# Optimization experiments

Measured on AMD Instinct MI355X. Metric: run time of the kernel, lower is better.

The kernel has to match this reference:

```python
import jax, jax.numpy as jnp
import numpy as np

# ---- hyperparameters (mirror the module's globals) ----
SZ      = 4096   # batch
SENLEN  = 128    # sentence length
VOCAB   = 50000  # len(wordVec)
DWE     = 100    # dimWE
MAXPOS  = 256    # MaxPos
DPE     = 5      # dimPE
DIMR    = 40     # dimR (event/role vocab)
DEE     = 32     # dimEE
DRE     = 16     # dimRE
MAXE    = 9      # maxE
DC      = 128    # dimC_arg
LOCLEN  = 16     # words in `loc` per sample
CIN     = DWE + 2 * DPE + DEE + (MAXE - 1) * DRE  # 270


def setup_inputs() -> dict:
    ks = jax.random.split(jax.random.key(0), 16)
    inp      = jax.random.randint(ks[0], (SZ, SENLEN), 0, VOCAB)
    pos1     = jax.random.randint(ks[1], (SZ, SENLEN), 0, MAXPOS)
    pos2     = jax.random.randint(ks[2], (SZ, SENLEN), 0, MAXPOS)
    loc      = jax.random.randint(ks[3], (SZ, LOCLEN), 0, VOCAB)
    # loc_mark in [1, 11] so indices 4:4+mark and 4+mark stay inside LOCLEN=16
    loc_mark = jax.random.randint(ks[4], (SZ,), 1, 12)
    subtype  = jax.random.randint(ks[5], (SZ,), 0, DIMR)
    argRole  = jax.random.randint(ks[6], (SZ, MAXE - 1), 0, DIMR)
    # binary piecewise masks (left / middle / right of the two anchors)
    maskL = (jax.random.uniform(ks[7], (SZ, SENLEN)) > 0.5).astype(jnp.float32)
    maskM = (jax.random.uniform(ks[8], (SZ, SENLEN)) > 0.5).astype(jnp.float32)
    maskR = (jax.random.uniform(ks[9], (SZ, SENLEN)) > 0.5).astype(jnp.float32)
    # learned parameters
    word_emb  = (jax.random.normal(ks[10], (VOCAB, DWE)) * 0.02).at[0].set(0.0)  # padding_idx=0
    pos_emb   = jax.random.normal(ks[11], (MAXPOS, DPE)) * 0.02
    event_emb = (jax.random.normal(ks[12], (DIMR, DEE)) * 0.02).at[0].set(0.0)
    role_emb  = (jax.random.normal(ks[13], (DIMR, DRE)) * 0.02).at[0].set(0.0)
    conv_w    = jax.random.normal(ks[14], (DC, CIN, 3)) * 0.02  # (out, in, k)
    conv_b    = jax.random.normal(ks[15], (DC,)) * 0.02
    return dict(inp=inp, pos1=pos1, pos2=pos2, loc=loc, loc_mark=loc_mark,
                subtype=subtype, argRole=argRole, maskL=maskL, maskM=maskM,
                maskR=maskR, word_emb=word_emb, pos_emb=pos_emb,
                event_emb=event_emb, role_emb=role_emb, conv_w=conv_w,
                conv_b=conv_b)


def reference(inp, pos1, pos2, loc, loc_mark, subtype, argRole,
              maskL, maskM, maskR, word_emb, pos_emb, event_emb, role_emb,
              conv_w, conv_b):
    sz = inp.shape[0]
    embeds = word_emb[inp]            # [SZ, S, DWE]
    p1 = pos_emb[pos1]                # [SZ, S, DPE]
    p2 = pos_emb[pos2]                # [SZ, S, DPE]

    # ---- vectorized ragged loc pooling (replaces the per-sample loop) ----
    loc_e = word_emb[loc]             # [SZ, LOCLEN, DWE]
    csum  = jnp.cumsum(loc_e, axis=1)
    # mean of loc_e[4 : 4+mark]  = (csum[3+mark] - csum[3]) / mark
    upper = jnp.take_along_axis(csum, (3 + loc_mark)[:, None, None], axis=1)[:, 0]
    mean4 = (upper - csum[:, 3]) / loc_mark[:, None].astype(loc_e.dtype)
    l5    = jnp.take_along_axis(loc_e, (4 + loc_mark)[:, None, None], axis=1)[:, 0]
    loc_embeds = jnp.concatenate(
        [loc_e[:, :4].reshape(sz, -1), mean4, l5], axis=1)  # [SZ, 6*DWE]

    # event / role embeddings broadcast across the sentence
    ev = jnp.broadcast_to(event_emb[subtype][:, None, :], (sz, SENLEN, DEE))
    rl = jnp.broadcast_to(role_emb[argRole].reshape(sz, 1, -1),
                          (sz, SENLEN, (MAXE - 1) * DRE))

    x = jnp.concatenate([embeds, p1, p2, ev, rl], axis=2)  # [SZ, S, CIN]
    x = jnp.transpose(x, (0, 2, 1))                         # [SZ, CIN, S]
    conved = jax.lax.conv_general_dilated(
        x, conv_w, window_strides=(1,), padding=[(1, 1)],
        dimension_numbers=('NCH', 'OIH', 'NCH')) + conv_b[None, :, None]

    def piece_pool(m):  # masked +1 then max over sentence
        return jnp.max(conved * m[:, None, :] + 1.0, axis=2)  # [SZ, DC]

    pooled = jnp.concatenate(
        [piece_pool(maskL), piece_pool(maskM), piece_pool(maskR)], axis=1) - 1.0
    rep = jnp.tanh(jnp.concatenate([pooled, loc_embeds], axis=1))  # dropout = identity (eval)
    return rep
```

## Files before the change

### kernel.cpp

```cpp
#include <hip/hip_runtime.h>
#include <hip/hip_bf16.h>

typedef unsigned short u16;
typedef __attribute__((ext_vector_type(8))) short bf16x8;
typedef __attribute__((ext_vector_type(4))) float f32x4;
typedef __attribute__((ext_vector_type(4))) int i32x4;
typedef __attribute__((ext_vector_type(2))) unsigned int u32x2;

constexpr int SEN  = 128;
constexpr int CIN  = 270;
constexpr int KA   = 352;
constexpr int NOUT = 984;
constexpr int XROW = 256;
constexpr int XTB  = 130 * XROW;
constexpr int WEBP = 256;
constexpr size_t WS_BASE = 90112 + 61440 + 491520;
constexpr size_t WS_NEED = WS_BASE + 50000ull * WEBP;

__device__ inline float ftanh(float x) {
    float e = __expf(2.0f * x);
    return 1.0f - 2.0f * __builtin_amdgcn_rcpf(e + 1.0f);
}
__device__ inline unsigned pk2(float x, float y) {
    union { __hip_bfloat162 h; unsigned u; } v;
    v.h = __float22bfloat162_rn(float2{x, y});
    return v.u;
}
__device__ __forceinline__ void gload_lds16(const void* g, void* l) {
    __builtin_amdgcn_global_load_lds(
        (const __attribute__((address_space(1))) void*)g,
        (__attribute__((address_space(3))) void*)l, 16, 0, 0);
}

__global__ void prep_all(const float* __restrict__ w, const float* __restrict__ ee,
                         const float* __restrict__ re, const int* __restrict__ loc,
                         const int* __restrict__ lmark, const float* __restrict__ we,
                         u16* __restrict__ Av, float* __restrict__ SE3,
                         float* __restrict__ SR3, u16* __restrict__ weB,
                         float* __restrict__ out) {
    const int b = blockIdx.x, tid = threadIdx.x;
    if (b < 176) {
        int i = b * 256 + tid;
        int dc = i / KA, K = i - dc * KA;
        int tap = (K >= 112) + (K >= 224) + (K >= 336);
        int ch  = K - 112 * tap;
        float v = (tap < 3 && ch < 110) ? w[(dc * CIN + ch) * 3 + tap] : 0.0f;
        union { __hip_bfloat16 h; u16 u; } cv;
        cv.h = __float2bfloat16(v);
        Av[i] = cv.u;
    } else if (b < 236) {
        int i = (b - 176) * 256 + tid;
        int k = i % 3, rest = i / 3;
        int dc = rest & 127, e = rest >> 7;
        float a = 0.f;
        for (int j = 0; j < 32; ++j)
            a += w[(dc * CIN + 110 + j) * 3 + k] * ee[e * 32 + j];
        SE3[i] = a;
    } else if (b < 716) {
        int i = (b - 236) * 256 + tid;
        int k = i % 3, rest = i / 3;
        int dc = rest & 127, rr = rest >> 7;
        int r = rr % 40, j = rr / 40;
        float a = 0.f;
        for (int d = 0; d < 16; ++d)
            a += w[(dc * CIN + 142 + j * 16 + d) * 3 + k] * re[r * 16 + d];
        SR3[i] = a;
    } else if (b < 2764) {
        int li = b - 716;
        int s = li * 2 + (tid >> 7);
        int d = tid & 127;
        if (d < 100) {
            const int* L = loc + (size_t)s * 16;
            float* o = out + (size_t)s * NOUT + 384;
#pragma unroll
            for (int i = 0; i < 4; ++i)
                o[i * 100 + d] = ftanh(we[(size_t)L[i] * 100 + d]);
            int mk = lmark[s];
            float acc = 0.f;
            for (int j = 0; j < mk; ++j)
                acc += we[(size_t)L[4 + j] * 100 + d];
            o[4 * 100 + d] = ftanh(acc / (float)mk);
            o[5 * 100 + d] = ftanh(we[(size_t)L[4 + mk] * 100 + d]);
        }
    } else {
        size_t i = (size_t)(b - 2764) * 256 + tid;
        int v  = (int)(i >> 6), cp = (int)(i & 63);
        int c0 = cp * 2;
        float x0 = (c0     < 100) ? we[(size_t)v * 100 + c0]     : 0.f;
        float x1 = (c0 + 1 < 100) ? we[(size_t)v * 100 + c0 + 1] : 0.f;
        ((unsigned*)weB)[(size_t)v * 64 + cp] = pk2(x0, x1);
    }
}

template <bool GLD>
__global__ __launch_bounds__(512)
__attribute__((amdgpu_waves_per_eu(4)))
void conv_pool(const int* __restrict__ inp, const int* __restrict__ pos1,
               const int* __restrict__ pos2, const int* __restrict__ subtype,
               const int* __restrict__ argRole,
               const float* __restrict__ maskL, const float* __restrict__ maskM,
               const float* __restrict__ maskR,
               const float* __restrict__ we, const float* __restrict__ pe,
               const float* __restrict__ cb,
               const u16* __restrict__ Av, const float* __restrict__ SE3,
               const float* __restrict__ SR3, const u16* __restrict__ weB,
               float* __restrict__ out)
{
    __shared__ __align__(16) char xT[2][XTB];
    __shared__ float sc[2][3 * 128];
    __shared__ float msk[2][3 * 128];

    const int tid  = threadIdx.x;
    const int lane = tid & 63;
    const int wid  = tid >> 6;
    const int cl   = lane & 15;
    const int rg   = lane >> 4;

    {
        i32x4 z = {0, 0, 0, 0};
        i32x4* pz = (i32x4*)xT;
#pragma unroll
        for (int i = 0; i < 9; ++i) {
            int o = tid + i * 512;
            if (o < 2 * XTB / 16) pz[o] = z;
        }
    }
    __syncthreads();

    const char* apBase = (const char*)Av + (wid * 16 + cl) * (KA * 2) + rg * 16;

    int addrB[11];
#pragma unroll
    for (int c = 0; c < 11; ++c) {
        int g   = 32 * c + 8 * rg;
        int tap = (g >= 112) + (g >= 224);
        int ch  = g - 112 * tap;
        int row0 = cl + tap;
        int phys = (ch >> 3) ^ (row0 & 15);
        addrB[c] = row0 * XROW + (phys << 4);
    }

    const int sbase = blockIdx.x * 8;

    float sk0 = 0.f, sk1 = 0.f, sk2 = 0.f;
    float cbv = (tid < 128) ? cb[tid] : 0.f;
    float pp[10];
#pragma unroll
    for (int i = 0; i < 10; ++i) pp[i] = 0.f;

    auto issueGather = [&](int s, char* xb, float* mb) {
#pragma unroll
        for (int q = 0; q < 4; ++q) {
            const int j   = (wid << 2) + q;
            const int tok = (j << 2) + (lane >> 4);
            const int idx = inp[s * SEN + tok];
            const int e   = (lane & 15) ^ ((tok + 1) & 15);
            const char* src = (const char*)weB + (size_t)idx * WEBP + (e << 4);
            gload_lds16(src, xb + XROW + (j << 10));
        }
        if (wid == 4) {
            const char* gL = (const char*)(maskL + (size_t)s * SEN);
            const char* gM = (const char*)(maskM + (size_t)s * SEN);
            const char* gR = (const char*)(maskR + (size_t)s * SEN);
            const char* s1 = (lane < 32) ? gL + (lane << 4)
                                         : gM + ((lane - 32) << 4);
            gload_lds16(s1, (char*)mb);
            if (lane < 32)
                gload_lds16(gR + (lane << 4), (char*)mb + 1024);
        }
    };

    auto smallLoad = [&](int s) {
        if (tid < 128) {
            int sub = subtype[s];
            i32x4 a0 = *(const i32x4*)(argRole + s * 8);
            i32x4 a1 = *(const i32x4*)(argRole + s * 8 + 4);
            int arr[8] = {a0[0], a0[1], a0[2], a0[3], a1[0], a1[1], a1[2], a1[3]};
            const float* bb = SE3 + (sub * 128 + tid) * 3;
            sk0 = bb[0]; sk1 = bb[1]; sk2 = bb[2];
#pragma unroll
            for (int j = 0; j < 8; ++j) {
                const float* rb = SR3 + ((j * 40 + arr[j]) * 128 + tid) * 3;
                sk0 += rb[0]; sk1 += rb[1]; sk2 += rb[2];
            }
        } else if (tid < 256) {
            int t = tid - 128;
            int p1 = pos1[s * SEN + t], p2 = pos2[s * SEN + t];
#pragma unroll
            for (int i = 0; i < 5; ++i) {
                pp[i]     = pe[p1 * 5 + i];
                pp[5 + i] = pe[p2 * 5 + i];
            }
        }
    };

    auto smallCommit = [&](int s, char* xb, float* scb, float* mb) {
        if (tid < 128) {
            scb[tid]       = sk0 + sk1 + sk2 + cbv;
            scb[128 + tid] = sk0;
            scb[256 + tid] = sk2;
        } else if (tid < 256) {
            int t = tid - 128, row = t + 1, rx = row & 15;
            u32x2 wa = { pk2(pp[0], pp[1]), pk2(pp[2], pp[3]) };
            *(u32x2*)(xb + row * XROW + ((12 ^ rx) << 4) + 8) = wa;
            union { bf16x8 v; unsigned u[4]; } wb;
            wb.u[0] = pk2(pp[4], pp[5]); wb.u[1] = pk2(pp[6], pp[7]);
            wb.u[2] = pk2(pp[8], pp[9]); wb.u[3] = 0;
            *(bf16x8*)(xb + row * XROW + ((13 ^ rx) << 4)) = wb.v;
        }
        if constexpr (!GLD) {
#pragma unroll
            for (int jj = 0; jj < 7; ++jj) {
                int q = tid + jj * 512;
                if (q < 3200) {
                    int tok = q / 25;
                    int e   = q - tok * 25;
                    int idx = inp[s * SEN + tok];
                    f32x4 v = *(const f32x4*)(we + (size_t)idx * 100 + e * 4);
                    int row  = tok + 1;
                    int phys = (e >> 1) ^ (row & 15);
                    u32x2 wv = { pk2(v[0], v[1]), pk2(v[2], v[3]) };
                    *(u32x2*)(xb + row * XROW + (phys << 4) + (e & 1) * 8) = wv;
                }
            }
            if (tid >= 256 && tid < 352) {
                int i = tid - 256;
                int m = i >> 5, j4 = i & 31;
                const float* msrc = (m == 0) ? maskL : (m == 1) ? maskM : maskR;
                *(f32x4*)(mb + m * 128 + j4 * 4) =
                    *(const f32x4*)(msrc + (size_t)s * SEN + j4 * 4);
            }
        }
    };

    smallLoad(sbase);
    if constexpr (GLD) issueGather(sbase, xT[0], msk[0]);
    __syncthreads();
    smallCommit(sbase, xT[0], sc[0], msk[0]);
    __syncthreads();

    for (int it = 0; it < 8; ++it) {
        const int s   = sbase + it;
        const int cur = it & 1;
        const char* xc = xT[cur];

        if (it < 7) {
            if constexpr (GLD) issueGather(s + 1, xT[cur ^ 1], msk[cur ^ 1]);
            smallLoad(s + 1);
        }

        const char* ap = apBase;
        asm volatile("" : "+v"(ap));

        f32x4 acc[8];
#pragma unroll
        for (int nf = 0; nf < 8; ++nf) acc[nf] = (f32x4){0.f, 0.f, 0.f, 0.f};

#pragma unroll
        for (int c = 0; c < 11; ++c) {
            const bf16x8 a = *(const bf16x8*)(ap + c * 64);
#pragma unroll
            for (int nf = 0; nf < 8; ++nf) {
                bf16x8 b = *(const bf16x8*)(xc + addrB[c] + nf * 4096);
                acc[nf] = __builtin_amdgcn_mfma_f32_16x16x32_bf16(
                    a, b, acc[nf], 0, 0, 0);
            }
        }

        const float* scc = sc[cur];
        const float* mc  = msk[cur];
        float sall[4], s0v[4], s2v[4];
#pragma unroll
        for (int r = 0; r < 4; ++r) {
            int dc = wid * 16 + rg * 4 + r;
            sall[r] = scc[dc]; s0v[r] = scc[128 + dc]; s2v[r] = scc[256 + dc];
        }
        float pm[3][4];
#pragma unroll
        for (int m = 0; m < 3; ++m)
#pragma unroll
            for (int r = 0; r < 4; ++r) pm[m][r] = -1e30f;

#pragma unroll
        for (int nf = 0; nf < 8; ++nf) {
            const int tt = nf * 16 + cl;
            const float m0 = mc[tt], m1 = mc[128 + tt], m2 = mc[256 + tt];
#pragma unroll
            for (int r = 0; r < 4; ++r) {
                float v = acc[nf][r] + sall[r];
                if (nf == 0) v -= (cl == 0)  ? s0v[r] : 0.f;
                if (nf == 7) v -= (cl == 15) ? s2v[r] : 0.f;
                pm[0][r] = fmaxf(pm[0][r], __builtin_fmaf(v, m0, 1.f));
                pm[1][r] = fmaxf(pm[1][r], __builtin_fmaf(v, m1, 1.f));
                pm[2][r] = fmaxf(pm[2][r], __builtin_fmaf(v, m2, 1.f));
            }
        }
#pragma unroll
        for (int m = 0; m < 3; ++m)
#pragma unroll
            for (int r = 0; r < 4; ++r)
#pragma unroll
                for (int d = 1; d < 16; d <<= 1)
                    pm[m][r] = fmaxf(pm[m][r], __shfl_xor(pm[m][r], d));
        if (cl < 3) {
            float* o = out + (size_t)s * NOUT + cl * 128 + wid * 16 + rg * 4;
#pragma unroll
            for (int r = 0; r < 4; ++r) {
                float v = (cl == 0) ? pm[0][r] : (cl == 1) ? pm[1][r] : pm[2][r];
                o[r] = ftanh(v - 1.f);
            }
        }

        __syncthreads();
        if (it < 7) smallCommit(s + 1, xT[cur ^ 1], sc[cur ^ 1], msk[cur ^ 1]);
        __syncthreads();
    }
}

extern "C" void kernel_launch(void* const* d_in, const int* in_sizes, int n_in,
                              void* d_out, int out_size, void* d_ws, size_t ws_size,
                              hipStream_t stream) {
    const int*   inp     = (const int*)d_in[0];
    const int*   pos1    = (const int*)d_in[1];
    const int*   pos2    = (const int*)d_in[2];
    const int*   loc     = (const int*)d_in[3];
    const int*   lmark   = (const int*)d_in[4];
    const int*   subtype = (const int*)d_in[5];
    const int*   argRole = (const int*)d_in[6];
    const float* maskL   = (const float*)d_in[7];
    const float* maskM   = (const float*)d_in[8];
    const float* maskR   = (const float*)d_in[9];
    const float* we      = (const float*)d_in[10];
    const float* pe      = (const float*)d_in[11];
    const float* ee      = (const float*)d_in[12];
    const float* re      = (const float*)d_in[13];
    const float* cw      = (const float*)d_in[14];
    const float* cb      = (const float*)d_in[15];
    float* out = (float*)d_out;

    char* ws = (char*)d_ws;
    u16*   Av  = (u16*)ws;
    float* SE3 = (float*)(ws + 90112);
    float* SR3 = (float*)(ws + 90112 + 61440);
    u16*   weB = (u16*)(ws + WS_BASE);

    const bool gld = (ws_size >= WS_NEED);
    const int prepGrid = gld ? 15264 : 2764;

    hipLaunchKernelGGL(prep_all, dim3(prepGrid), dim3(256), 0, stream,
                       cw, ee, re, loc, lmark, we, Av, SE3, SR3, weB, out);
    if (gld) {
        hipLaunchKernelGGL((conv_pool<true>), dim3(512), dim3(512), 0, stream,
                           inp, pos1, pos2, subtype, argRole, maskL, maskM, maskR,
                           we, pe, cb, Av, SE3, SR3, weB, out);
    } else {
        hipLaunchKernelGGL((conv_pool<false>), dim3(512), dim3(512), 0, stream,
                           inp, pos1, pos2, subtype, argRole, maskL, maskM, maskR,
                           we, pe, cb, Av, SE3, SR3, weB, out);
    }
}
```

Baseline: 97.80 us.

## Restructure conv GEMM to 32x32x16 MFMA with tokens as A operand

Switches the conv GEMM from 16x16x32 MFMAs (weights as A, tokens as B, each wave owning 16 output channels across all tokens) to 32x32x16 MFMAs where each wave owns 32 tokens by 64 channels, with the activation tile as the A operand. Weights are re-laid-out in prep so they are streamed from global/L2 per k-step. The piecewise max-pool now reduces partially per wave and then combines four token-quarters through a new shared-memory buffer before tanh and store. This aims to cut LDS reads per MFMA and the shuffle-heavy reduction, at the cost of an extra LDS buffer and a cross-wave reduction step.

```diff
diff --git a/kernel.cpp b/kernel.cpp
--- a/kernel.cpp
+++ b/kernel.cpp
@@ -4,12 +4,12 @@
 typedef unsigned short u16;
 typedef __attribute__((ext_vector_type(8))) short bf16x8;
 typedef __attribute__((ext_vector_type(4))) float f32x4;
+typedef __attribute__((ext_vector_type(16))) float f32x16;
 typedef __attribute__((ext_vector_type(4))) int i32x4;
 typedef __attribute__((ext_vector_type(2))) unsigned int u32x2;
 
 constexpr int SEN  = 128;
 constexpr int CIN  = 270;
-constexpr int KA   = 352;
 constexpr int NOUT = 984;
 constexpr int XROW = 256;
 constexpr int XTB  = 130 * XROW;
@@ -35,19 +35,22 @@
 __global__ void prep_all(const float* __restrict__ w, const float* __restrict__ ee,
                          const float* __restrict__ re, const int* __restrict__ loc,
                          const int* __restrict__ lmark, const float* __restrict__ we,
-                         u16* __restrict__ Av, float* __restrict__ SE3,
+                         u16* __restrict__ WB, float* __restrict__ SE3,
                          float* __restrict__ SR3, u16* __restrict__ weB,
                          float* __restrict__ out) {
     const int b = blockIdx.x, tid = threadIdx.x;
     if (b < 176) {
         int i = b * 256 + tid;
-        int dc = i / KA, K = i - dc * KA;
-        int tap = (K >= 112) + (K >= 224) + (K >= 336);
-        int ch  = K - 112 * tap;
-        float v = (tap < 3 && ch < 110) ? w[(dc * CIN + ch) * 3 + tap] : 0.0f;
+        int kg = i >> 10;
+        int dc = (i >> 3) & 127;
+        int j  = i & 7;
+        int g  = kg * 8 + j;
+        int tap = (g >= 112) + (g >= 224);
+        int ch  = g - 112 * tap;
+        float v = (g < 336 && ch < 110) ? w[(dc * CIN + ch) * 3 + tap] : 0.0f;
         union { __hip_bfloat16 h; u16 u; } cv;
         cv.h = __float2bfloat16(v);
-        Av[i] = cv.u;
+        WB[i] = cv.u;
     } else if (b < 236) {
         int i = (b - 176) * 256 + tid;
         int k = i % 3, rest = i / 3;
@@ -93,8 +96,7 @@
 }
 
 template <bool GLD>
-__global__ __launch_bounds__(512)
-__attribute__((amdgpu_waves_per_eu(4)))
+__global__ __launch_bounds__(512, 4)
 void conv_pool(const int* __restrict__ inp, const int* __restrict__ pos1,
                const int* __restrict__ pos2, const int* __restrict__ subtype,
                const int* __restrict__ argRole,
@@ -102,19 +104,22 @@
                const float* __restrict__ maskR,
                const float* __restrict__ we, const float* __restrict__ pe,
                const float* __restrict__ cb,
-               const u16* __restrict__ Av, const float* __restrict__ SE3,
+               const u16* __restrict__ WB, const float* __restrict__ SE3,
                const float* __restrict__ SR3, const u16* __restrict__ weB,
                float* __restrict__ out)
 {
     __shared__ __align__(16) char xT[2][XTB];
     __shared__ float sc[2][3 * 128];
     __shared__ float msk[2][3 * 128];
+    __shared__ float part[12 * 128];
 
     const int tid  = threadIdx.x;
     const int lane = tid & 63;
     const int wid  = tid >> 6;
-    const int cl   = lane & 15;
-    const int rg   = lane >> 4;
+    const int l31  = lane & 31;
+    const int hi   = lane >> 5;
+    const int q    = wid >> 1;
+    const int dch  = wid & 1;
 
     {
         i32x4 z = {0, 0, 0, 0};
@@ -127,18 +132,17 @@
     }
     __syncthreads();
 
-    const char* apBase = (const char*)Av + (wid * 16 + cl) * (KA * 2) + rg * 16;
-
-    int addrB[11];
-#pragma unroll
-    for (int c = 0; c < 11; ++c) {
-        int g   = 32 * c + 8 * rg;
-        int tap = (g >= 112) + (g >= 224);
-        int ch  = g - 112 * tap;
-        int row0 = cl + tap;
-        int phys = (ch >> 3) ^ (row0 & 15);
-        addrB[c] = row0 * XROW + (phys << 4);
-    }
+    int addrA[22];
+#pragma unroll
+    for (int ks = 0; ks < 22; ++ks) {
+        int tap = (ks >= 7) + (ks >= 14);
+        int c0  = ks * 2 - 14 * tap;
+        int row = q * 32 + l31 + tap;
+        int slot = (c0 + hi) ^ (row & 15);
+        addrA[ks] = row * XROW + (slot << 4);
+    }
+
+    const char* wpBase = (const char*)WB + hi * 2048 + ((dch * 64 + l31) << 4);
 
     const int sbase = blockIdx.x * 8;
 
@@ -150,8 +154,8 @@
 
     auto issueGather = [&](int s, char* xb, float* mb) {
 #pragma unroll
-        for (int q = 0; q < 4; ++q) {
-            const int j   = (wid << 2) + q;
+        for (int qq = 0; qq < 4; ++qq) {
+            const int j   = (wid << 2) + qq;
             const int tok = (j << 2) + (lane >> 4);
             const int idx = inp[s * SEN + tok];
             const int e   = (lane & 15) ^ ((tok + 1) & 15);
@@ -211,10 +215,10 @@
         if constexpr (!GLD) {
 #pragma unroll
             for (int jj = 0; jj < 7; ++jj) {
-                int q = tid + jj * 512;
-                if (q < 3200) {
-                    int tok = q / 25;
-                    int e   = q - tok * 25;
+                int qf = tid + jj * 512;
+                if (qf < 3200) {
+                    int tok = qf / 25;
+                    int e   = qf - tok * 25;
                     int idx = inp[s * SEN + tok];
                     f32x4 v = *(const f32x4*)(we + (size_t)idx * 100 + e * 4);
                     int row  = tok + 1;
@@ -249,69 +253,72 @@
             smallLoad(s + 1);
         }
 
-        const char* ap = apBase;
-        asm volatile("" : "+v"(ap));
-
-        f32x4 acc[8];
-#pragma unroll
-        for (int nf = 0; nf < 8; ++nf) acc[nf] = (f32x4){0.f, 0.f, 0.f, 0.f};
-
-#pragma unroll
-        for (int c = 0; c < 11; ++c) {
-            const bf16x8 a = *(const bf16x8*)(ap + c * 64);
-#pragma unroll
-            for (int nf = 0; nf < 8; ++nf) {
-                bf16x8 b = *(const bf16x8*)(xc + addrB[c] + nf * 4096);
-                acc[nf] = __builtin_amdgcn_mfma_f32_16x16x32_bf16(
-                    a, b, acc[nf], 0, 0, 0);
-            }
+        const char* wp = wpBase;
+        asm volatile("" : "+v"(wp));
+
+        f32x16 acc0, acc1;
+#pragma unroll
+        for (int r = 0; r < 16; ++r) { acc0[r] = 0.f; acc1[r] = 0.f; }
+
+#pragma unroll
+        for (int ks = 0; ks < 22; ++ks) {
+            bf16x8 xa = *(const bf16x8*)(xc + addrA[ks]);
+            bf16x8 w0 = *(const bf16x8*)(wp + ks * 4096);
+            bf16x8 w1 = *(const bf16x8*)(wp + ks * 4096 + 512);
+            acc0 = __builtin_amdgcn_mfma_f32_32x32x16_bf16(xa, w0, acc0, 0, 0, 0);
+            acc1 = __builtin_amdgcn_mfma_f32_32x32x16_bf16(xa, w1, acc1, 0, 0, 0);
         }
 
         const float* scc = sc[cur];
         const float* mc  = msk[cur];
-        float sall[4], s0v[4], s2v[4];
-#pragma unroll
-        for (int r = 0; r < 4; ++r) {
-            int dc = wid * 16 + rg * 4 + r;
-            sall[r] = scc[dc]; s0v[r] = scc[128 + dc]; s2v[r] = scc[256 + dc];
-        }
-        float pm[3][4];
-#pragma unroll
-        for (int m = 0; m < 3; ++m)
-#pragma unroll
-            for (int r = 0; r < 4; ++r) pm[m][r] = -1e30f;
-
-#pragma unroll
-        for (int nf = 0; nf < 8; ++nf) {
-            const int tt = nf * 16 + cl;
-            const float m0 = mc[tt], m1 = mc[128 + tt], m2 = mc[256 + tt];
-#pragma unroll
-            for (int r = 0; r < 4; ++r) {
-                float v = acc[nf][r] + sall[r];
-                if (nf == 0) v -= (cl == 0)  ? s0v[r] : 0.f;
-                if (nf == 7) v -= (cl == 15) ? s2v[r] : 0.f;
-                pm[0][r] = fmaxf(pm[0][r], __builtin_fmaf(v, m0, 1.f));
-                pm[1][r] = fmaxf(pm[1][r], __builtin_fmaf(v, m1, 1.f));
-                pm[2][r] = fmaxf(pm[2][r], __builtin_fmaf(v, m2, 1.f));
-            }
-        }
-#pragma unroll
-        for (int m = 0; m < 3; ++m)
-#pragma unroll
-            for (int r = 0; r < 4; ++r)
-#pragma unroll
-                for (int d = 1; d < 16; d <<= 1)
-                    pm[m][r] = fmaxf(pm[m][r], __shfl_xor(pm[m][r], d));
-        if (cl < 3) {
-            float* o = out + (size_t)s * NOUT + cl * 128 + wid * 16 + rg * 4;
-#pragma unroll
-            for (int r = 0; r < 4; ++r) {
-                float v = (cl == 0) ? pm[0][r] : (cl == 1) ? pm[1][r] : pm[2][r];
-                o[r] = ftanh(v - 1.f);
+        const int dc0 = dch * 64 + l31;
+        const int dc1 = dc0 + 32;
+        const float sall0 = scc[dc0], sall1 = scc[dc1];
+
+        float v0[16], v1[16];
+#pragma unroll
+        for (int r = 0; r < 16; ++r) {
+            v0[r] = acc0[r] + sall0;
+            v1[r] = acc1[r] + sall1;
+        }
+        if (q == 0 && lane < 32) {
+            v0[0] -= scc[128 + dc0];
+            v1[0] -= scc[128 + dc1];
+        }
+        if (q == 3 && lane >= 32) {
+            v0[15] -= scc[256 + dc0];
+            v1[15] -= scc[256 + dc1];
+        }
+
+#pragma unroll
+        for (int m = 0; m < 3; ++m) {
+            float pm0 = -1e30f, pm1 = -1e30f;
+#pragma unroll
+            for (int g = 0; g < 4; ++g) {
+                f32x4 mk = *(const f32x4*)(mc + m * 128 + q * 32 + g * 8 + hi * 4);
+#pragma unroll
+                for (int j = 0; j < 4; ++j) {
+                    int r = g * 4 + j;
+                    pm0 = fmaxf(pm0, __builtin_fmaf(v0[r], mk[j], 1.f));
+                    pm1 = fmaxf(pm1, __builtin_fmaf(v1[r], mk[j], 1.f));
+                }
+            }
+            pm0 = fmaxf(pm0, __shfl_xor(pm0, 32));
+            pm1 = fmaxf(pm1, __shfl_xor(pm1, 32));
+            if (lane < 32) {
+                part[(m * 4 + q) * 128 + dc0] = pm0;
+                part[(m * 4 + q) * 128 + dc1] = pm1;
             }
         }
 
         __syncthreads();
+
+        if (tid < 384) {
+            int m = tid >> 7, dc = tid & 127;
+            const float* pb = part + m * 4 * 128 + dc;
+            float v = fmaxf(fmaxf(pb[0], pb[128]), fmaxf(pb[256], pb[384]));
+            out[(size_t)s * NOUT + m * 128 + dc] = ftanh(v - 1.f);
+        }
         if (it < 7) smallCommit(s + 1, xT[cur ^ 1], sc[cur ^ 1], msk[cur ^ 1]);
         __syncthreads();
     }
@@ -339,7 +346,7 @@
     float* out = (float*)d_out;
 
     char* ws = (char*)d_ws;
-    u16*   Av  = (u16*)ws;
+    u16*   WB  = (u16*)ws;
     float* SE3 = (float*)(ws + 90112);
     float* SR3 = (float*)(ws + 90112 + 61440);
     u16*   weB = (u16*)(ws + WS_BASE);
@@ -348,14 +355,14 @@
     const int prepGrid = gld ? 15264 : 2764;
 
     hipLaunchKernelGGL(prep_all, dim3(prepGrid), dim3(256), 0, stream,
-                       cw, ee, re, loc, lmark, we, Av, SE3, SR3, weB, out);
+                       cw, ee, re, loc, lmark, we, WB, SE3, SR3, weB, out);
     if (gld) {
         hipLaunchKernelGGL((conv_pool<true>), dim3(512), dim3(512), 0, stream,
                            inp, pos1, pos2, subtype, argRole, maskL, maskM, maskR,
-                           we, pe, cb, Av, SE3, SR3, weB, out);
+                           we, pe, cb, WB, SE3, SR3, weB, out);
     } else {
         hipLaunchKernelGGL((conv_pool<false>), dim3(512), dim3(512), 0, stream,
                            inp, pos1, pos2, subtype, argRole, maskL, maskM, maskR,
-                           we, pe, cb, Av, SE3, SR3, weB, out);
-    }
-}
+                           we, pe, cb, WB, SE3, SR3, weB, out);
+    }
+}
```

Measured after the change: 98.11 us. Within noise of the previous version (+0.3%).
